# Kernel optimization log

Measured on AMD Instinct MI355X. Metric: run time of the kernel, lower is better.

## Reference

```python
import jax, jax.numpy as jnp
import numpy as np

NUM_CLASSES = 81
THRESHOLD = 0.5
NEGPOS_RATIO = 3
VAR0, VAR1 = 0.1, 0.2
B, P, T = 64, 25000, 16


def setup_inputs() -> dict:
    key = jax.random.key(0)
    k1, k2, k3, k4, k5, k6 = jax.random.split(key, 6)
    loc_data = jax.random.normal(k1, (B, P, 4), dtype=jnp.float32)
    conf_data = jax.random.normal(k2, (B, P, NUM_CLASSES), dtype=jnp.float32)
    # priors in center-offset form (cx, cy, w, h), all in (0,1), w/h > 0
    centers = jax.random.uniform(k3, (P, 2), minval=0.05, maxval=0.95)
    wh = jax.random.uniform(k4, (P, 2), minval=0.05, maxval=0.3)
    priors = jnp.concatenate([centers, wh], axis=1).astype(jnp.float32)
    # ground-truth boxes in corner form (xmin, ymin, xmax, ymax), valid (max > min)
    pts = jax.random.uniform(k5, (B, T, 2, 2), minval=0.0, maxval=0.98)
    mn = jnp.min(pts, axis=2)
    mx = jnp.max(pts, axis=2) + 0.02  # strictly positive width/height
    boxes = jnp.concatenate([mn, jnp.clip(mx, 0.0, 1.0)], axis=-1)
    labels = jax.random.randint(k6, (B, T), 0, NUM_CLASSES - 1).astype(jnp.float32)
    targets = jnp.concatenate([boxes, labels[..., None]], axis=-1)
    return {"loc_data": loc_data, "conf_data": conf_data, "priors": priors, "targets": targets}


def point_form(p):
    # (cx,cy,w,h) -> (xmin,ymin,xmax,ymax)
    return jnp.concatenate([p[:, :2] - p[:, 2:] / 2, p[:, :2] + p[:, 2:] / 2], axis=1)


def jaccard(a, b):
    # a: [T,4], b: [P,4], corner form -> IoU [T,P]
    lt = jnp.maximum(a[:, None, :2], b[None, :, :2])
    rb = jnp.minimum(a[:, None, 2:], b[None, :, 2:])
    wh = jnp.clip(rb - lt, 0.0)
    inter = wh[..., 0] * wh[..., 1]
    area_a = ((a[:, 2] - a[:, 0]) * (a[:, 3] - a[:, 1]))[:, None]
    area_b = ((b[:, 2] - b[:, 0]) * (b[:, 3] - b[:, 1]))[None, :]
    return inter / (area_a + area_b - inter)


def encode(matched, priors):
    # SSD offset encoding with variances
    g_cxcy = ((matched[:, :2] + matched[:, 2:]) * 0.5 - priors[:, :2]) / (VAR0 * priors[:, 2:])
    g_wh = jnp.log((matched[:, 2:] - matched[:, :2]) / priors[:, 2:]) / VAR1
    return jnp.concatenate([g_cxcy, g_wh], axis=1)


def match_one(truths, labels, priors):
    # truths: [T,4] corner, labels: [T], priors: [P,4] center
    overlaps = jaccard(truths, point_form(priors))        # [T,P]
    best_prior_idx = jnp.argmax(overlaps, axis=1)         # [T]
    best_truth_overlap = jnp.max(overlaps, axis=0)        # [P]
    best_truth_idx = jnp.argmax(overlaps, axis=0)         # [P]
    best_truth_overlap = best_truth_overlap.at[best_prior_idx].set(2.0)
    for j in range(T):
        best_truth_idx = best_truth_idx.at[best_prior_idx[j]].set(j)
    matched = truths[best_truth_idx]                      # [P,4]
    conf = labels[best_truth_idx].astype(jnp.int32) + 1
    conf = jnp.where(best_truth_overlap < THRESHOLD, 0, conf)
    return encode(matched, priors), conf


def smooth_l1(d):
    ad = jnp.abs(d)
    return jnp.where(ad < 1.0, 0.5 * d * d, ad - 0.5)


def reference(loc_data, conf_data, priors, targets):
    truths = jax.lax.stop_gradient(targets[..., :4])  # .data in torch
    labels = jax.lax.stop_gradient(targets[..., 4])
    loc_t, conf_t = jax.vmap(match_one, in_axes=(0, 0, None))(truths, labels, priors)
    pos = conf_t > 0                                      # [B,P]
    num_priors = pos.shape[1]
    # localization: smooth-L1 summed over positive priors (masked instead of boolean gather)
    loss_l = jnp.sum(jnp.where(pos[..., None], smooth_l1(loc_data - loc_t), 0.0))
    # per-prior conf loss = logsumexp - logit[target]
    lse = jax.nn.logsumexp(conf_data, axis=-1)            # [B,P]
    conf_gt = jnp.take_along_axis(conf_data, conf_t[..., None], axis=-1)[..., 0]
    ce = lse - conf_gt
    # hard negative mining: zero positives, double argsort rank
    loss_c = jnp.where(pos, 0.0, ce)
    loss_idx = jnp.argsort(-loss_c, axis=1)
    idx_rank = jnp.argsort(loss_idx, axis=1)
    num_pos = jnp.sum(pos, axis=1, keepdims=True)
    num_neg = jnp.minimum(NEGPOS_RATIO * num_pos, num_priors - 1)
    neg = idx_rank < num_neg
    # cross-entropy summed over positives + mined negatives
    loss_conf = jnp.sum(jnp.where(pos | neg, ce, 0.0))
    N = jnp.maximum(jnp.sum(num_pos).astype(loc_data.dtype), 1.0)
    return loss_l / N, loss_conf / N
```

## Files before the change

### kernel.cpp

```cpp
#include <hip/hip_runtime.h>

namespace {

constexpr int kB = 64;
constexpr int kP = 25000;
constexpr int kT = 16;
constexpr int kC = 81;
constexpr int kRowsPerBlk = 64;
constexpr int kChunks = 16;
constexpr int kChunkP = (kP + kChunks - 1) / kChunks;
constexpr float kThresh = 0.5f;

__device__ __forceinline__ float smooth_l1(float d) {
  float ad = fabsf(d);
  return ad < 1.0f ? 0.5f * d * d : ad - 0.5f;
}

__global__ __launch_bounds__(256) void match1_kernel(
    const float* __restrict__ priors,
    const float* __restrict__ targets,
    unsigned char* __restrict__ mcode,
    unsigned long long* __restrict__ best_prior) {
  const int chunk = blockIdx.x;
  const int b = blockIdx.y;
  const int tid = threadIdx.x;
  const int p0 = chunk * kChunkP;
  const int p1 = min(p0 + kChunkP, kP);

  __shared__ float tx0[kT], ty0[kT], tx1[kT], ty1[kT], tarea[kT];
  __shared__ float smax[kT][256];
  __shared__ int sidx[kT][256];

  if (tid < kT) {
    const float* tg = targets + (b * kT + tid) * 5;
    float x0 = tg[0], y0 = tg[1], x1 = tg[2], y1 = tg[3];
    tx0[tid] = x0; ty0[tid] = y0; tx1[tid] = x1; ty1[tid] = y1;
    tarea[tid] = (x1 - x0) * (y1 - y0);
  }
  __syncthreads();

  float bestv[kT];
  int besti[kT];
#pragma unroll
  for (int t = 0; t < kT; ++t) { bestv[t] = -1.0f; besti[t] = 0; }

  for (int p = p0 + tid; p < p1; p += 256) {
    float4 pr = reinterpret_cast<const float4*>(priors)[p];
    float px0 = pr.x - pr.z * 0.5f, py0 = pr.y - pr.w * 0.5f;
    float px1 = pr.x + pr.z * 0.5f, py1 = pr.y + pr.w * 0.5f;
    float parea = (px1 - px0) * (py1 - py0);
    float mv = -1.0f;
    int mt = 0;
#pragma unroll
    for (int t = 0; t < kT; ++t) {
      float lx = fmaxf(tx0[t], px0), ly = fmaxf(ty0[t], py0);
      float rx = fminf(tx1[t], px1), ry = fminf(ty1[t], py1);
      float w = fmaxf(rx - lx, 0.0f), h = fmaxf(ry - ly, 0.0f);
      float inter = w * h;
      float iou = inter / (tarea[t] + parea - inter);
      if (iou > bestv[t]) { bestv[t] = iou; besti[t] = p; }
      if (iou > mv) { mv = iou; mt = t; }
    }
    mcode[b * kP + p] = (unsigned char)(mt | (mv < kThresh ? 0x80 : 0));
  }
#pragma unroll
  for (int t = 0; t < kT; ++t) { smax[t][tid] = bestv[t]; sidx[t][tid] = besti[t]; }
  __syncthreads();
  for (int s = 128; s > 0; s >>= 1) {
    if (tid < s) {
#pragma unroll
      for (int t = 0; t < kT; ++t) {
        float v1 = smax[t][tid], v2 = smax[t][tid + s];
        int i1 = sidx[t][tid], i2 = sidx[t][tid + s];
        if (v2 > v1 || (v2 == v1 && i2 < i1)) { smax[t][tid] = v2; sidx[t][tid] = i2; }
      }
    }
    __syncthreads();
  }
  if (tid < kT) {
    unsigned long long pk = ((unsigned long long)__float_as_uint(smax[tid][0]) << 32) |
                            (unsigned long long)(0xFFFFFFFFu - (unsigned)sidx[tid][0]);
    atomicMax(&best_prior[b * kT + tid], pk);
  }
}

__global__ __launch_bounds__(256) void match2_kernel(
    const float* __restrict__ loc_data,
    const float* __restrict__ priors,
    const float* __restrict__ targets,
    const unsigned long long* __restrict__ best_prior,
    unsigned char* __restrict__ code,
    int* __restrict__ num_pos,
    float* __restrict__ loss_l_acc) {
  const int chunk = blockIdx.x;
  const int b = blockIdx.y;
  const int tid = threadIdx.x;
  const int p0 = chunk * kChunkP;
  const int p1 = min(p0 + kChunkP, kP);

  __shared__ int s_bp[kT];
  __shared__ float sx0[kT], sy0[kT], sx1[kT], sy1[kT], slab[kT];
  __shared__ float swf[4];
  __shared__ int swi[4];

  if (tid < kT) {
    s_bp[tid] = (int)(0xFFFFFFFFu -
                      (unsigned)(best_prior[b * kT + tid] & 0xFFFFFFFFull));
    const float* tg = targets + (b * kT + tid) * 5;
    sx0[tid] = tg[0]; sy0[tid] = tg[1]; sx1[tid] = tg[2]; sy1[tid] = tg[3];
    slab[tid] = tg[4];
  }
  __syncthreads();

  float lsum = 0.0f;
  int pcount = 0;
  for (int p = p0 + tid; p < p1; p += 256) {
    int c = code[b * kP + p];
    int mt = c & 0x0F;
    bool neg = (c & 0x80) != 0;
    bool forced = false;
#pragma unroll
    for (int j = 0; j < kT; ++j) {
      if (s_bp[j] == p) { mt = j; forced = true; }
    }
    int conf = (!forced && neg) ? 0 : ((int)slab[mt] + 1);
    code[b * kP + p] = (unsigned char)conf;
    if (conf > 0) {
      ++pcount;
      float4 pr = reinterpret_cast<const float4*>(priors)[p];
      float mx0 = sx0[mt], my0 = sy0[mt], mx1 = sx1[mt], my1 = sy1[mt];
      float gcx = ((mx0 + mx1) * 0.5f - pr.x) / (0.1f * pr.z);
      float gcy = ((my0 + my1) * 0.5f - pr.y) / (0.1f * pr.w);
      float gw = logf((mx1 - mx0) / pr.z) / 0.2f;
      float gh = logf((my1 - my0) / pr.w) / 0.2f;
      float4 ld = reinterpret_cast<const float4*>(loc_data)[b * kP + p];
      lsum += smooth_l1(ld.x - gcx) + smooth_l1(ld.y - gcy) +
              smooth_l1(ld.z - gw) + smooth_l1(ld.w - gh);
    }
  }
  for (int off = 32; off > 0; off >>= 1) {
    lsum += __shfl_down(lsum, off, 64);
    pcount += __shfl_down(pcount, off, 64);
  }
  if ((tid & 63) == 0) { swf[tid >> 6] = lsum; swi[tid >> 6] = pcount; }
  __syncthreads();
  if (tid == 0) {
    float lt = swf[0] + swf[1] + swf[2] + swf[3];
    int pt = swi[0] + swi[1] + swi[2] + swi[3];
    if (lt != 0.0f) atomicAdd(loss_l_acc, lt);
    if (pt != 0) atomicAdd(&num_pos[b], pt);
  }
}

__global__ __launch_bounds__(256) void ce_kernel(
    const float* __restrict__ conf_data,
    const unsigned char* __restrict__ conf_t,
    float* __restrict__ loss_c,
    float* __restrict__ pos_ce_acc) {
  __shared__ float tile[kRowsPerBlk * kC];
  __shared__ float swsum[4];
  const int tid = threadIdx.x;
  const long long base = (long long)blockIdx.x * (kRowsPerBlk * kC);
  const float4* src = reinterpret_cast<const float4*>(conf_data + base);
  float4* dst = reinterpret_cast<float4*>(tile);
#pragma unroll
  for (int i = 0; i < 6; ++i) {
    int idx = tid + i * 256;
    if (idx < kRowsPerBlk * kC / 4) dst[idx] = src[idx];
  }
  __syncthreads();

  const int r = tid >> 2;
  const int sub = tid & 3;
  const float* x = tile + r * kC;
  float m = -3.0e38f;
  for (int j = sub; j < kC; j += 4) m = fmaxf(m, x[j]);
  m = fmaxf(m, __shfl_xor(m, 1, 64));
  m = fmaxf(m, __shfl_xor(m, 2, 64));
  float s = 0.0f;
  for (int j = sub; j < kC; j += 4) s += __expf(x[j] - m);
  s += __shfl_xor(s, 1, 64);
  s += __shfl_xor(s, 2, 64);
  float posce = 0.0f;
  if (sub == 0) {
    const long long row = (long long)blockIdx.x * kRowsPerBlk + r;
    float lse = __logf(s) + m;
    int ct = conf_t[row];
    float ce = lse - x[ct];
    bool pos = ct > 0;
    loss_c[row] = pos ? 0.0f : ce;
    posce = pos ? ce : 0.0f;
  }
  for (int off = 32; off > 0; off >>= 1) posce += __shfl_down(posce, off, 64);
  if ((tid & 63) == 0) swsum[tid >> 6] = posce;
  __syncthreads();
  if (tid == 0) {
    float t = swsum[0] + swsum[1] + swsum[2] + swsum[3];
    if (t != 0.0f) atomicAdd(pos_ce_acc, t);
  }
}

__global__ __launch_bounds__(256) void select_kernel(
    const float* __restrict__ loss_c,
    const int* __restrict__ num_pos,
    float* __restrict__ neg_ce_acc) {
  const int b = blockIdx.x;
  const int tid = threadIdx.x;
  const int k = min(3 * num_pos[b], kP - 1);
  __shared__ int swi[4];
  __shared__ float swf[4];
  if (k <= 0) return;

  constexpr int kV4 = kP / 4;
  constexpr int kPer = (kV4 + 255) / 256;
  const float4* v4 = reinterpret_cast<const float4*>(loss_c + (long long)b * kP);
  float4 lv[kPer];
#pragma unroll
  for (int j = 0; j < kPer; ++j) {
    int i = tid + j * 256;
    lv[j] = (i < kV4) ? v4[i] : float4{0.0f, 0.0f, 0.0f, 0.0f};
  }

  unsigned int ans = 0;
  for (int bit = 30; bit >= 0; --bit) {
    const unsigned int cand = ans | (1u << bit);
    int cnt = 0;
#pragma unroll
    for (int j = 0; j < kPer; ++j) {
      cnt += (__float_as_uint(lv[j].x) >= cand) + (__float_as_uint(lv[j].y) >= cand) +
             (__float_as_uint(lv[j].z) >= cand) + (__float_as_uint(lv[j].w) >= cand);
    }
    for (int off = 32; off > 0; off >>= 1) cnt += __shfl_down(cnt, off, 64);
    if ((tid & 63) == 0) swi[tid >> 6] = cnt;
    __syncthreads();
    int tot = swi[0] + swi[1] + swi[2] + swi[3];
    if (tot >= k) ans = cand;
    __syncthreads();
  }
  float sum = 0.0f;
  int cgt = 0;
#pragma unroll
  for (int j = 0; j < kPer; ++j) {
    if (__float_as_uint(lv[j].x) > ans) { sum += lv[j].x; ++cgt; }
    if (__float_as_uint(lv[j].y) > ans) { sum += lv[j].y; ++cgt; }
    if (__float_as_uint(lv[j].z) > ans) { sum += lv[j].z; ++cgt; }
    if (__float_as_uint(lv[j].w) > ans) { sum += lv[j].w; ++cgt; }
  }
  for (int off = 32; off > 0; off >>= 1) {
    sum += __shfl_down(sum, off, 64);
    cgt += __shfl_down(cgt, off, 64);
  }
  if ((tid & 63) == 0) { swf[tid >> 6] = sum; swi[tid >> 6] = cgt; }
  __syncthreads();
  if (tid == 0) {
    float st = swf[0] + swf[1] + swf[2] + swf[3];
    int ct = swi[0] + swi[1] + swi[2] + swi[3];
    atomicAdd(neg_ce_acc, st + (float)(k - ct) * __uint_as_float(ans));
  }
}

__global__ void finalize_kernel(const int* __restrict__ num_pos,
                                const float* __restrict__ acc,
                                float* __restrict__ out) {
  int tid = threadIdx.x;
  int np = num_pos[tid];
  for (int off = 32; off > 0; off >>= 1) np += __shfl_down(np, off, 64);
  if (tid == 0) {
    float N = fmaxf((float)np, 1.0f);
    out[0] = acc[0] / N;
    out[1] = (acc[1] + acc[2]) / N;
  }
}

}

extern "C" void kernel_launch(void* const* d_in, const int* in_sizes, int n_in,
                              void* d_out, int out_size, void* d_ws, size_t ws_size,
                              hipStream_t stream) {
  const float* loc_data = (const float*)d_in[0];
  const float* conf_data = (const float*)d_in[1];
  const float* priors = (const float*)d_in[2];
  const float* targets = (const float*)d_in[3];
  float* out = (float*)d_out;

  char* ws = (char*)d_ws;
  float* loss_c = (float*)ws;
  unsigned char* code = (unsigned char*)(ws + 6400000);
  unsigned long long* best_prior = (unsigned long long*)(ws + 8000000);
  int* num_pos = (int*)(ws + 8008192);
  float* acc = (float*)(ws + 8008448);

  hipMemsetAsync(ws + 8000000, 0, 8512, stream);
  hipLaunchKernelGGL(match1_kernel, dim3(kChunks, kB), dim3(256), 0, stream,
                     priors, targets, code, best_prior);
  hipLaunchKernelGGL(match2_kernel, dim3(kChunks, kB), dim3(256), 0, stream,
                     loc_data, priors, targets, best_prior, code, num_pos, acc + 0);
  hipLaunchKernelGGL(ce_kernel, dim3(kB * kP / kRowsPerBlk), dim3(256), 0, stream,
                     conf_data, code, loss_c, acc + 1);
  hipLaunchKernelGGL(select_kernel, dim3(kB), dim3(256), 0, stream,
                     loss_c, num_pos, acc + 2);
  hipLaunchKernelGGL(finalize_kernel, dim3(1), dim3(64), 0, stream,
                     num_pos, acc, out);
}
```

Before: 834.4 us.

## Rewrite CE kernel as wave-per-row grid-stride loop without shared tile

Replaces the shared-memory tiled cross-entropy kernel with a fixed grid where each wave processes a contiguous range of rows, loading 81 logits across lanes and reducing via shuffles. The target logit is fetched by a lane shuffle and the positive-CE accumulation is done per wave with one atomic. It also drops the max subtraction in logsumexp, removing a reduction pass but risking overflow for large logits. Per-row serial latency may limit memory-level parallelism.

```diff
diff --git a/kernel.cpp b/kernel.cpp
--- a/kernel.cpp
+++ b/kernel.cpp
@@ -6,10 +6,10 @@
 constexpr int kP = 25000;
 constexpr int kT = 16;
 constexpr int kC = 81;
-constexpr int kRowsPerBlk = 64;
 constexpr int kChunks = 16;
 constexpr int kChunkP = (kP + kChunks - 1) / kChunks;
 constexpr float kThresh = 0.5f;
+constexpr int kCeBlocks = 4096;
 
 __device__ __forceinline__ float smooth_l1(float d) {
   float ad = fabsf(d);
@@ -157,47 +157,32 @@
     const unsigned char* __restrict__ conf_t,
     float* __restrict__ loss_c,
     float* __restrict__ pos_ce_acc) {
-  __shared__ float tile[kRowsPerBlk * kC];
-  __shared__ float swsum[4];
-  const int tid = threadIdx.x;
-  const long long base = (long long)blockIdx.x * (kRowsPerBlk * kC);
-  const float4* src = reinterpret_cast<const float4*>(conf_data + base);
-  float4* dst = reinterpret_cast<float4*>(tile);
-#pragma unroll
-  for (int i = 0; i < 6; ++i) {
-    int idx = tid + i * 256;
-    if (idx < kRowsPerBlk * kC / 4) dst[idx] = src[idx];
-  }
-  __syncthreads();
-
-  const int r = tid >> 2;
-  const int sub = tid & 3;
-  const float* x = tile + r * kC;
-  float m = -3.0e38f;
-  for (int j = sub; j < kC; j += 4) m = fmaxf(m, x[j]);
-  m = fmaxf(m, __shfl_xor(m, 1, 64));
-  m = fmaxf(m, __shfl_xor(m, 2, 64));
-  float s = 0.0f;
-  for (int j = sub; j < kC; j += 4) s += __expf(x[j] - m);
-  s += __shfl_xor(s, 1, 64);
-  s += __shfl_xor(s, 2, 64);
+  const int tid = threadIdx.x;
+  const int lane = tid & 63;
+  const long long nrows = (long long)kB * kP;
+  const long long nwaves = (long long)gridDim.x * 4;
+  const long long gw = (long long)blockIdx.x * 4 + (tid >> 6);
+  const long long chunk = (nrows + nwaves - 1) / nwaves;
+  const long long r0 = gw * chunk;
+  const long long r1 = min(r0 + chunk, nrows);
+
   float posce = 0.0f;
-  if (sub == 0) {
-    const long long row = (long long)blockIdx.x * kRowsPerBlk + r;
-    float lse = __logf(s) + m;
+  for (long long row = r0; row < r1; ++row) {
+    const float* x = conf_data + row * kC;
+    float v1 = x[lane];
+    float v2 = (lane < kC - 64) ? x[64 + lane] : 0.0f;
+    float e = __expf(v1) + ((lane < kC - 64) ? __expf(v2) : 0.0f);
+    for (int off = 32; off > 0; off >>= 1) e += __shfl_down(e, off, 64);
     int ct = conf_t[row];
-    float ce = lse - x[ct];
-    bool pos = ct > 0;
-    loss_c[row] = pos ? 0.0f : ce;
-    posce = pos ? ce : 0.0f;
-  }
-  for (int off = 32; off > 0; off >>= 1) posce += __shfl_down(posce, off, 64);
-  if ((tid & 63) == 0) swsum[tid >> 6] = posce;
-  __syncthreads();
-  if (tid == 0) {
-    float t = swsum[0] + swsum[1] + swsum[2] + swsum[3];
-    if (t != 0.0f) atomicAdd(pos_ce_acc, t);
-  }
+    float xgt = (ct < 64) ? __shfl(v1, ct, 64) : __shfl(v2, ct - 64, 64);
+    if (lane == 0) {
+      float ce = __logf(e) - xgt;
+      bool pos = ct > 0;
+      loss_c[row] = pos ? 0.0f : ce;
+      posce += pos ? ce : 0.0f;
+    }
+  }
+  if (lane == 0 && posce != 0.0f) atomicAdd(pos_ce_acc, posce);
 }
 
 __global__ __launch_bounds__(256) void select_kernel(
@@ -295,7 +280,7 @@
                      priors, targets, code, best_prior);
   hipLaunchKernelGGL(match2_kernel, dim3(kChunks, kB), dim3(256), 0, stream,
                      loc_data, priors, targets, best_prior, code, num_pos, acc + 0);
-  hipLaunchKernelGGL(ce_kernel, dim3(kB * kP / kRowsPerBlk), dim3(256), 0, stream,
+  hipLaunchKernelGGL(ce_kernel, dim3(kCeBlocks), dim3(256), 0, stream,
                      conf_data, code, loss_c, acc + 1);
   hipLaunchKernelGGL(select_kernel, dim3(kB), dim3(256), 0, stream,
                      loss_c, num_pos, acc + 2);
```

Result: slower. 929.9 us (+11.4%).
